# Kernel tuning notes

Measured on AMD Instinct MI355X. Metric: run time of the kernel, lower is better.

The kernel has to match this reference:

```python
import jax, jax.numpy as jnp
import numpy as np

N = 32768   # nodes
D = 16      # fixed in-degree (neighbors per node)
C = 128     # in_channels
H = 128     # hidden_channels (out of each SAGEConv)


def setup_inputs() -> dict:
    key = jax.random.key(0)
    ks = jax.random.split(key, 20)
    x = jax.random.normal(ks[0], (N, C), dtype=jnp.float32)
    # edges sorted by destination, exactly D neighbors per node (PyG
    # LSTMAggregation requires dst-sorted edge_index)
    src = jax.random.randint(ks[1], (N * D,), 0, N, dtype=jnp.int32)
    dst = jnp.repeat(jnp.arange(N, dtype=jnp.int32), D)
    edge_index = jnp.stack([src, dst])  # [2, E]

    s = 1.0 / np.sqrt(C)
    def mat(k, o, i):
        return jax.random.uniform(k, (o, i), jnp.float32, -s, s)
    def vec(k, o):
        return jax.random.uniform(k, (o,), jnp.float32, -s, s)

    inp = {"x": x, "edge_index": edge_index}
    for k0, base in [(2, "conv1"), (10, "conv2")]:
        inp[f"{base}_wih"] = mat(ks[k0 + 0], 4 * C, C)   # LSTM input weights
        inp[f"{base}_whh"] = mat(ks[k0 + 1], 4 * C, C)   # LSTM hidden weights
        inp[f"{base}_bih"] = vec(ks[k0 + 2], 4 * C)
        inp[f"{base}_bhh"] = vec(ks[k0 + 3], 4 * C)
        inp[f"{base}_wl"] = mat(ks[k0 + 4], H, C)        # lin_l (neighbor branch, has bias)
        inp[f"{base}_bl"] = vec(ks[k0 + 5], H)
        inp[f"{base}_wr"] = mat(ks[k0 + 6], H, C)        # lin_r (root branch, no bias)
    return inp


def _lstm_last(seq, wih, whh, bih, bhh):
    # seq: [D, N, C]. PyTorch LSTM, gate order (i, f, g, o).
    # PyG LSTMAggregation returns lstm(x)[0][:, -1] == hidden state at the
    # last (padded) timestep; here every node has exactly D real neighbors.
    n = seq.shape[1]
    h0 = jnp.zeros((n, wih.shape[0] // 4), seq.dtype)
    b = bih + bhh

    def step(carry, x_t):
        h, c = carry
        g = x_t @ wih.T + h @ whh.T + b            # [N, 4H]
        i, f, gg, o = jnp.split(g, 4, axis=-1)
        c = jax.nn.sigmoid(f) * c + jax.nn.sigmoid(i) * jnp.tanh(gg)
        h = jax.nn.sigmoid(o) * jnp.tanh(c)
        return (h, c), None

    (h, _), _ = jax.lax.scan(step, (h0, h0), seq)
    return h


def _sage_conv(x, src, wih, whh, bih, bhh, wl, bl, wr):
    n, c = x.shape
    d = src.shape[0] // n
    # dense neighbor batch [N, D, C]: edges are dst-sorted with fixed degree,
    # so the gather reshapes directly (== PyG to_dense_batch)
    msgs = x[src].reshape(n, d, c)
    aggr = _lstm_last(jnp.swapaxes(msgs, 0, 1), wih, whh, bih, bhh)  # [N, C]
    return aggr @ wl.T + bl + x @ wr.T


def reference(x, edge_index,
              conv1_wih, conv1_whh, conv1_bih, conv1_bhh, conv1_wl, conv1_bl, conv1_wr,
              conv2_wih, conv2_whh, conv2_bih, conv2_bhh, conv2_wl, conv2_bl, conv2_wr):
    src = edge_index[0]
    h = _sage_conv(x, src, conv1_wih, conv1_whh, conv1_bih, conv1_bhh,
                   conv1_wl, conv1_bl, conv1_wr)
    h = jax.nn.relu(h)
    out = _sage_conv(h, src, conv2_wih, conv2_whh, conv2_bih, conv2_bhh,
                     conv2_wl, conv2_bl, conv2_wr)
    return out
```

## Files before the change

### kernel.cpp

```cpp
#include <hip/hip_runtime.h>
#include <stdint.h>

#define NN 32768
#define DEG 16
#define CH 128
#define G4 512
#define MB 128
#define BUF 32768

typedef short bf16x8 __attribute__((ext_vector_type(8)));
typedef float f32x4 __attribute__((ext_vector_type(4)));
typedef unsigned short u16;
typedef u16 u16x8 __attribute__((ext_vector_type(8)));
typedef uint32_t u32;

#define L2E  1.4426950408889634f
#define L2E2 2.8853900817779268f

__device__ __forceinline__ u16 f2bf(float f) {
  union { float f; uint32_t u; } v; v.f = f;
  uint32_t u = v.u;
  return (u16)((u + 0x7FFFu + ((u >> 16) & 1u)) >> 16);
}
__device__ __forceinline__ float exp2f_fast(float x) {
#if __has_builtin(__builtin_amdgcn_exp2f)
  return __builtin_amdgcn_exp2f(x);
#else
  float r; asm("v_exp_f32 %0, %1" : "=v"(r) : "v"(x)); return r;
#endif
}
__device__ __forceinline__ float rcpf_fast(float x) {
#if __has_builtin(__builtin_amdgcn_rcpf)
  return __builtin_amdgcn_rcpf(x);
#else
  float r; asm("v_rcp_f32 %0, %1" : "=v"(r) : "v"(x)); return r;
#endif
}
__device__ __forceinline__ u32 cvtpk(float lo, float hi) {
  u32 r; asm("v_cvt_pk_bf16_f32 %0, %1, %2" : "=v"(r) : "v"(lo), "v"(hi));
  return r;
}

__global__ void k_cvt_bf16(const float* __restrict__ in, u16* __restrict__ out, int n8) {
  int i = blockIdx.x * blockDim.x + threadIdx.x;
  if (i >= n8) return;
  const float* pp = in + (size_t)i * 8;
  u16x8 o;
  #pragma unroll
  for (int j = 0; j < 8; ++j) o[j] = f2bf(pp[j]);
  *(u16x8*)(out + (size_t)i * 8) = o;
}

__global__ void k_pack_lstm(const float* __restrict__ wih, const float* __restrict__ whh,
                            const float* __restrict__ bih, const float* __restrict__ bhh,
                            u16* __restrict__ Wc, float* __restrict__ bs) {
  int idx = blockIdx.x * blockDim.x + threadIdx.x;
  int g = idx >> 8, k = idx & 255;
  int gate = g >> 7;
  float sc = (gate == 2) ? L2E2 : L2E;
  float v = (k < CH) ? wih[g * CH + k] : whh[g * CH + (k - CH)];
  Wc[g * 256 + k] = f2bf(v * sc);
  if (k == 0) bs[g] = (bih[g] + bhh[g]) * sc;
}

__global__ void k_pack_lin(const float* __restrict__ wl, const float* __restrict__ wr,
                           u16* __restrict__ W) {
  int idx = blockIdx.x * blockDim.x + threadIdx.x;
  int o = idx >> 8, k = idx & 255;
  float v = (k < CH) ? wl[o * CH + k] : wr[o * CH + (k - CH)];
  W[o * 256 + k] = f2bf(v);
}

__global__ __launch_bounds__(512, 2)
void k_gates(const u16* __restrict__ xin, const u16* __restrict__ Wc,
             u16* __restrict__ gx) {
  const int lane = threadIdx.x & 63;
  const int wave = threadIdx.x >> 6;
  const int l15 = lane & 15, lg = lane >> 4;
  const int nodeBase = blockIdx.x * 64;

  bf16x8 B[4][4];
  int cb[4];
  #pragma unroll
  for (int ct = 0; ct < 4; ++ct) {
    int j = (wave * 4 + ct) * 16 + l15;
    int wr = ((j & 3) << 7) + (j >> 2);
    cb[ct] = (j >> 2) * 8 + (j & 3) * 2;
    #pragma unroll
    for (int kt = 0; kt < 4; ++kt)
      B[ct][kt] = *(const bf16x8*)(Wc + wr * 256 + kt * 32 + lg * 8);
  }
  char* gxc = (char*)gx;
  const f32x4 zero4 = {0.f, 0.f, 0.f, 0.f};
  #pragma unroll
  for (int mt = 0; mt < 4; ++mt) {
    bf16x8 A[4];
    #pragma unroll
    for (int kt = 0; kt < 4; ++kt)
      A[kt] = *(const bf16x8*)(xin + (size_t)(nodeBase + mt * 16 + l15) * CH + kt * 32 + lg * 8);
    f32x4 acc[4] = { zero4, zero4, zero4, zero4 };
    #pragma unroll
    for (int kt = 0; kt < 4; ++kt)
      #pragma unroll
      for (int ct = 0; ct < 4; ++ct)
        acc[ct] = __builtin_amdgcn_mfma_f32_16x16x32_bf16(A[kt], B[ct][kt], acc[ct], 0, 0, 0);
    #pragma unroll
    for (int ct = 0; ct < 4; ++ct)
      #pragma unroll
      for (int q = 0; q < 4; ++q)
        *(u16*)(gxc + (size_t)(nodeBase + mt * 16 + lg * 4 + q) * 1024 + cb[ct]) =
            f2bf(acc[ct][q]);
  }
}

#define GXISSUE(m) do {                                                        \
    int4 sv_ = *(const int4*)(ldsc + sTr + (m) * 64);                          \
    gq[m][0] = *(const uint2*)(gxb + (((u32)sv_.x << 10) + gxoff));            \
    gq[m][1] = *(const uint2*)(gxb + (((u32)sv_.y << 10) + gxoff));            \
    gq[m][2] = *(const uint2*)(gxb + (((u32)sv_.z << 10) + gxoff));            \
    gq[m][3] = *(const uint2*)(gxb + (((u32)sv_.w << 10) + gxoff));            \
  } while (0)

__global__ __launch_bounds__(512, 2)
void k_lstm(const u16* __restrict__ gx, const int* __restrict__ src,
            const u16* __restrict__ Wc, const float* __restrict__ bs,
            u16* __restrict__ aggr) {
  __shared__ char lds[2 * 32768 + 8192];
  char* ldsc = lds;
  const int tid = threadIdx.x;
  const int lane = tid & 63;
  const int wave = tid >> 6;
  const int l15 = lane & 15;
  const int lg  = lane >> 4;
  const int nodeBase = blockIdx.x * MB;

  {
    int row = tid >> 2, tq = (tid & 3) * 4;
    int4 s4 = *(const int4*)(src + (size_t)(nodeBase + row) * DEG + tq);
    int b = 65536 + row * 4;
    *(int*)(ldsc + b + (tq + 0) * 512) = s4.x;
    *(int*)(ldsc + b + (tq + 1) * 512) = s4.y;
    *(int*)(ldsc + b + (tq + 2) * 512) = s4.z;
    *(int*)(ldsc + b + (tq + 3) * 512) = s4.w;
  }
  {
    int4 z = {0, 0, 0, 0};
    #pragma unroll
    for (int j = 0; j < 4; ++j) *(int4*)(ldsc + tid * 64 + j * 16) = z;
  }

  bf16x8 Wf[4][4];
  {
    const u16* wp = Wc + (wave * 16 + l15) * 256 + 128 + lg * 8;
    #pragma unroll
    for (int gt = 0; gt < 4; ++gt)
      #pragma unroll
      for (int kt = 0; kt < 4; ++kt)
        Wf[gt][kt] = *(const bf16x8*)(wp + gt * (CH * 256) + kt * 32);
  }
  f32x4 bias[4];
  #pragma unroll
  for (int gt = 0; gt < 4; ++gt) {
    float b = bs[gt * CH + wave * 16 + l15];
    bias[gt] = { b, b, b, b };
  }

  int aAr = l15 * 256 + ((lg * 16) ^ ((l15 & 7) << 4));
  int aBr = aAr ^ 64;
  const int hcol = (wave * 16 + l15) * 2;
  int hw0 = (lg * 4 + 0) * 256 + (hcol ^ ((((lg * 4) + 0) & 7) << 4)) + BUF;
  int hw1 = (lg * 4 + 1) * 256 + (hcol ^ ((((lg * 4) + 1) & 7) << 4)) + BUF;
  int hw2 = (lg * 4 + 2) * 256 + (hcol ^ ((((lg * 4) + 2) & 7) << 4)) + BUF;
  int hw3 = (lg * 4 + 3) * 256 + (hcol ^ ((((lg * 4) + 3) & 7) << 4)) + BUF;
  int sTr = 65536 + lg * 16;
  const u32 gxoff = (u32)(wave * 16 + l15) * 8;
  const char* gxb = (const char*)gx;
  u16* aggrp = aggr + (size_t)(nodeBase + lg * 4) * CH + wave * 16 + l15;

  float cst[8][4] = {{0.f}};
  f32x4 acc[2][4];

  __syncthreads();

  #pragma unroll 1
  for (int t = 0; t < DEG; ++t) {
    __syncthreads();
    uint2 gq[8][4];
    GXISSUE(0); GXISSUE(1); GXISSUE(2);
    #pragma unroll
    for (int mt = 0; mt < 8; ++mt) {
      const int pp = mt & 1;
      if (mt < 5) GXISSUE(mt + 3);
      __builtin_amdgcn_s_setprio(1);
      {
        const bf16x8 A0 = *(const bf16x8*)(ldsc + aAr + mt * 4096);
        const bf16x8 A1 = *(const bf16x8*)(ldsc + aBr + mt * 4096);
        const bf16x8 A2 = *(const bf16x8*)(ldsc + aAr + mt * 4096 + 128);
        const bf16x8 A3 = *(const bf16x8*)(ldsc + aBr + mt * 4096 + 128);
        #pragma unroll
        for (int gt = 0; gt < 4; ++gt)
          acc[pp][gt] = __builtin_amdgcn_mfma_f32_16x16x32_bf16(A0, Wf[gt][0], bias[gt], 0, 0, 0);
        #pragma unroll
        for (int gt = 0; gt < 4; ++gt)
          acc[pp][gt] = __builtin_amdgcn_mfma_f32_16x16x32_bf16(A1, Wf[gt][1], acc[pp][gt], 0, 0, 0);
        #pragma unroll
        for (int gt = 0; gt < 4; ++gt)
          acc[pp][gt] = __builtin_amdgcn_mfma_f32_16x16x32_bf16(A2, Wf[gt][2], acc[pp][gt], 0, 0, 0);
        #pragma unroll
        for (int gt = 0; gt < 4; ++gt)
          acc[pp][gt] = __builtin_amdgcn_mfma_f32_16x16x32_bf16(A3, Wf[gt][3], acc[pp][gt], 0, 0, 0);
      }
      __builtin_amdgcn_s_setprio(0);
      float hq[4];
      #pragma unroll
      for (int q = 0; q < 4; ++q) {
        float xi = __uint_as_float(gq[mt][q].x << 16);
        float xf = __uint_as_float(gq[mt][q].x & 0xFFFF0000u);
        float xg = __uint_as_float(gq[mt][q].y << 16);
        float xo = __uint_as_float(gq[mt][q].y & 0xFFFF0000u);
        float p0 = acc[pp][0][q] + xi;
        float p1 = acc[pp][1][q] + xf;
        float p2 = acc[pp][2][q] + xg;
        float p3 = acc[pp][3][q] + xo;
        float si = rcpf_fast(1.0f + exp2f_fast(-p0));
        float sf = rcpf_fast(1.0f + exp2f_fast(-p1));
        float so = rcpf_fast(1.0f + exp2f_fast(-p3));
        float gg = fmaf(-2.0f, rcpf_fast(1.0f + exp2f_fast(p2)), 1.0f);
        float c  = fmaf(sf, cst[mt][q], si * gg);
        cst[mt][q] = c;
        float tc = fmaf(-2.0f, rcpf_fast(1.0f + exp2f_fast(c * L2E2)), 1.0f);
        hq[q] = so * tc;
      }
      u32 hp0 = cvtpk(hq[0], hq[1]);
      u32 hp1 = cvtpk(hq[2], hq[3]);
      if (t != DEG - 1) {
        *(u16*)(ldsc + hw0 + mt * 4096) = (u16)hp0;
        *(u16*)(ldsc + hw1 + mt * 4096) = (u16)(hp0 >> 16);
        *(u16*)(ldsc + hw2 + mt * 4096) = (u16)hp1;
        *(u16*)(ldsc + hw3 + mt * 4096) = (u16)(hp1 >> 16);
      } else {
        u16* op_ = aggrp + mt * 16 * CH;
        op_[0 * CH] = (u16)hp0;
        op_[1 * CH] = (u16)(hp0 >> 16);
        op_[2 * CH] = (u16)hp1;
        op_[3 * CH] = (u16)(hp1 >> 16);
      }
    }
    aAr ^= BUF; aBr ^= BUF;
    hw0 ^= BUF; hw1 ^= BUF; hw2 ^= BUF; hw3 ^= BUF;
    sTr += 512;
  }
}

__global__ __launch_bounds__(256, 4)
void k_linear(const u16* __restrict__ aggr, const u16* __restrict__ xroot,
              const u16* __restrict__ W, const float* __restrict__ bl,
              u16* __restrict__ out_bf, float* __restrict__ out_f, int relu) {
  const int lane = threadIdx.x & 63;
  const int wave = threadIdx.x >> 6;
  const int l15 = lane & 15, lg = lane >> 4;
  const int rowBase = blockIdx.x * 64 + wave * 16;

  f32x4 acc[8];
  #pragma unroll
  for (int nt = 0; nt < 8; ++nt) {
    float b = bl[nt * 16 + l15];
    acc[nt] = { b, b, b, b };
  }
  #pragma unroll
  for (int kt = 0; kt < 8; ++kt) {
    const u16* ap = (kt < 4) ? (aggr  + (size_t)(rowBase + l15) * CH + kt * 32 + lg * 8)
                             : (xroot + (size_t)(rowBase + l15) * CH + (kt - 4) * 32 + lg * 8);
    bf16x8 A = *(const bf16x8*)ap;
    #pragma unroll
    for (int nt = 0; nt < 8; ++nt) {
      bf16x8 B = *(const bf16x8*)(W + (nt * 16 + l15) * 256 + kt * 32 + lg * 8);
      acc[nt] = __builtin_amdgcn_mfma_f32_16x16x32_bf16(A, B, acc[nt], 0, 0, 0);
    }
  }
  #pragma unroll
  for (int nt = 0; nt < 8; ++nt) {
    #pragma unroll
    for (int q = 0; q < 4; ++q) {
      float v = acc[nt][q];
      if (relu) v = fmaxf(v, 0.0f);
      int row = rowBase + lg * 4 + q;
      int col = nt * 16 + l15;
      if (out_bf) out_bf[(size_t)row * CH + col] = f2bf(v);
      else        out_f[(size_t)row * CH + col]  = v;
    }
  }
}

extern "C" void kernel_launch(void* const* d_in, const int* in_sizes, int n_in,
                              void* d_out, int out_size, void* d_ws, size_t ws_size,
                              hipStream_t stream) {
  (void)in_sizes; (void)n_in; (void)out_size; (void)ws_size;
  const float* x    = (const float*)d_in[0];
  const int*   ei   = (const int*)d_in[1];
  const float* w1ih = (const float*)d_in[2];
  const float* w1hh = (const float*)d_in[3];
  const float* b1ih = (const float*)d_in[4];
  const float* b1hh = (const float*)d_in[5];
  const float* w1l  = (const float*)d_in[6];
  const float* b1l  = (const float*)d_in[7];
  const float* w1r  = (const float*)d_in[8];
  const float* w2ih = (const float*)d_in[9];
  const float* w2hh = (const float*)d_in[10];
  const float* b2ih = (const float*)d_in[11];
  const float* b2hh = (const float*)d_in[12];
  const float* w2l  = (const float*)d_in[13];
  const float* b2l  = (const float*)d_in[14];
  const float* w2r  = (const float*)d_in[15];

  char* p = (char*)d_ws;
  u16* x_bf  = (u16*)p;  p += (size_t)NN * CH * 2;
  u16* h1_bf = (u16*)p;  p += (size_t)NN * CH * 2;
  u16* ag_bf = (u16*)p;  p += (size_t)NN * CH * 2;
  u16* Wc1   = (u16*)p;  p += G4 * 256 * 2;
  u16* Wc2   = (u16*)p;  p += G4 * 256 * 2;
  u16* Wl1   = (u16*)p;  p += CH * 256 * 2;
  u16* Wl2   = (u16*)p;  p += CH * 256 * 2;
  float* bs1 = (float*)p; p += G4 * 4;
  float* bs2 = (float*)p; p += G4 * 4;
  u16* Gx    = (u16*)p;  p += (size_t)NN * G4 * 2;

  k_cvt_bf16<<<(NN * CH / 8 + 255) / 256, 256, 0, stream>>>(x, x_bf, NN * CH / 8);
  k_pack_lstm<<<G4, 256, 0, stream>>>(w1ih, w1hh, b1ih, b1hh, Wc1, bs1);
  k_pack_lstm<<<G4, 256, 0, stream>>>(w2ih, w2hh, b2ih, b2hh, Wc2, bs2);
  k_pack_lin<<<CH, 256, 0, stream>>>(w1l, w1r, Wl1);
  k_pack_lin<<<CH, 256, 0, stream>>>(w2l, w2r, Wl2);

  k_gates<<<NN / 64, 512, 0, stream>>>(x_bf, Wc1, Gx);
  k_lstm<<<NN / MB, 512, 0, stream>>>(Gx, ei, Wc1, bs1, ag_bf);
  k_linear<<<NN / 64, 256, 0, stream>>>(ag_bf, x_bf, Wl1, b1l, h1_bf, nullptr, 1);
  k_gates<<<NN / 64, 512, 0, stream>>>(h1_bf, Wc2, Gx);
  k_lstm<<<NN / MB, 512, 0, stream>>>(Gx, ei, Wc2, bs2, ag_bf);
  k_linear<<<NN / 64, 256, 0, stream>>>(ag_bf, h1_bf, Wl2, b2l, nullptr, (float*)d_out, 0);
}
```

Measured before the change: 331.7 us.

## Halve LSTM block tile, raise occupancy, prefetch gate gathers across steps

The LSTM kernel now processes 64 nodes per block instead of 128, with half the LDS footprint and launch bounds raised to 4 blocks per SM. It also software-pipelines the gathered input-gate loads one step ahead, including across timesteps. The input-gate bias is folded into the gates GEMM so the per-step accumulator starts from the gathered gate values, and the five prep kernels are merged into a single launch. The aim is better latency hiding for the recurrent step and the random gathers. In exchange there is more register pressure and each block's weight-fragment load is amortized over fewer nodes.

```diff
diff --git a/kernel.cpp b/kernel.cpp
--- a/kernel.cpp
+++ b/kernel.cpp
@@ -4,9 +4,8 @@
 #define NN 32768
 #define DEG 16
 #define CH 128
-#define G4 512
-#define MB 128
-#define BUF 32768
+#define MB 64
+#define BUF 16384
 
 typedef short bf16x8 __attribute__((ext_vector_type(8)));
 typedef float f32x4 __attribute__((ext_vector_type(4)));
@@ -26,14 +25,14 @@
 #if __has_builtin(__builtin_amdgcn_exp2f)
   return __builtin_amdgcn_exp2f(x);
 #else
-  float r; asm("v_exp_f32 %0, %1" : "=v"(r) : "v"(x)); return r;
+  float r; asm volatile("v_exp_f32 %0, %1\n\ts_nop 0" : "=v"(r) : "v"(x)); return r;
 #endif
 }
 __device__ __forceinline__ float rcpf_fast(float x) {
 #if __has_builtin(__builtin_amdgcn_rcpf)
   return __builtin_amdgcn_rcpf(x);
 #else
-  float r; asm("v_rcp_f32 %0, %1" : "=v"(r) : "v"(x)); return r;
+  float r; asm volatile("v_rcp_f32 %0, %1\n\ts_nop 0" : "=v"(r) : "v"(x)); return r;
 #endif
 }
 __device__ __forceinline__ u32 cvtpk(float lo, float hi) {
@@ -41,64 +40,81 @@
   return r;
 }
 
-__global__ void k_cvt_bf16(const float* __restrict__ in, u16* __restrict__ out, int n8) {
-  int i = blockIdx.x * blockDim.x + threadIdx.x;
-  if (i >= n8) return;
-  const float* pp = in + (size_t)i * 8;
-  u16x8 o;
-  #pragma unroll
-  for (int j = 0; j < 8; ++j) o[j] = f2bf(pp[j]);
-  *(u16x8*)(out + (size_t)i * 8) = o;
-}
-
-__global__ void k_pack_lstm(const float* __restrict__ wih, const float* __restrict__ whh,
-                            const float* __restrict__ bih, const float* __restrict__ bhh,
-                            u16* __restrict__ Wc, float* __restrict__ bs) {
-  int idx = blockIdx.x * blockDim.x + threadIdx.x;
-  int g = idx >> 8, k = idx & 255;
-  int gate = g >> 7;
-  float sc = (gate == 2) ? L2E2 : L2E;
-  float v = (k < CH) ? wih[g * CH + k] : whh[g * CH + (k - CH)];
-  Wc[g * 256 + k] = f2bf(v * sc);
-  if (k == 0) bs[g] = (bih[g] + bhh[g]) * sc;
-}
-
-__global__ void k_pack_lin(const float* __restrict__ wl, const float* __restrict__ wr,
-                           u16* __restrict__ W) {
-  int idx = blockIdx.x * blockDim.x + threadIdx.x;
-  int o = idx >> 8, k = idx & 255;
-  float v = (k < CH) ? wl[o * CH + k] : wr[o * CH + (k - CH)];
-  W[o * 256 + k] = f2bf(v);
+__global__ void k_prep(const float* __restrict__ x, u16* __restrict__ x_bf,
+    const float* __restrict__ w1ih, const float* __restrict__ w1hh,
+    const float* __restrict__ b1ih, const float* __restrict__ b1hh,
+    u16* __restrict__ Wc1, float* __restrict__ bs1,
+    const float* __restrict__ w2ih, const float* __restrict__ w2hh,
+    const float* __restrict__ b2ih, const float* __restrict__ b2hh,
+    u16* __restrict__ Wc2, float* __restrict__ bs2,
+    const float* __restrict__ w1l, const float* __restrict__ w1r, u16* __restrict__ Wl1,
+    const float* __restrict__ w2l, const float* __restrict__ w2r, u16* __restrict__ Wl2) {
+  const int bid = blockIdx.x, tid = threadIdx.x;
+  {
+    int i = bid * 256 + tid;
+    const float* pp = x + (size_t)i * 8;
+    u16x8 o;
+    #pragma unroll
+    for (int j = 0; j < 8; ++j) o[j] = f2bf(pp[j]);
+    *(u16x8*)(x_bf + (size_t)i * 8) = o;
+  }
+  if (bid < 1024) {
+    const int b2 = bid >= 512;
+    const float* wih = b2 ? w2ih : w1ih;
+    const float* whh = b2 ? w2hh : w1hh;
+    const float* bih = b2 ? b2ih : b1ih;
+    const float* bhh = b2 ? b2hh : b1hh;
+    u16* Wc = b2 ? Wc2 : Wc1;
+    float* bsp = b2 ? bs2 : bs1;
+    int idx = (bid & 511) * 256 + tid;
+    int g = idx >> 8, k = idx & 255;
+    float sc = ((g >> 7) == 2) ? L2E2 : L2E;
+    float v = (k < CH) ? wih[g * CH + k] : whh[g * CH + (k - CH)];
+    Wc[g * 256 + k] = f2bf(v * sc);
+    if (k == 0) bsp[g] = (bih[g] + bhh[g]) * sc;
+  } else if (bid < 1280) {
+    const int b2 = bid >= 1152;
+    const float* wl = b2 ? w2l : w1l;
+    const float* wr = b2 ? w2r : w1r;
+    u16* W = b2 ? Wl2 : Wl1;
+    int idx = ((bid - 1024) & 127) * 256 + tid;
+    int o = idx >> 8, k = idx & 255;
+    float v = (k < CH) ? wl[o * CH + k] : wr[o * CH + (k - CH)];
+    W[o * 256 + k] = f2bf(v);
+  }
 }
 
 __global__ __launch_bounds__(512, 2)
 void k_gates(const u16* __restrict__ xin, const u16* __restrict__ Wc,
-             u16* __restrict__ gx) {
+             const float* __restrict__ bs, u16* __restrict__ gx) {
   const int lane = threadIdx.x & 63;
   const int wave = threadIdx.x >> 6;
   const int l15 = lane & 15, lg = lane >> 4;
   const int nodeBase = blockIdx.x * 64;
 
   bf16x8 B[4][4];
+  float bv[4];
   int cb[4];
   #pragma unroll
   for (int ct = 0; ct < 4; ++ct) {
     int j = (wave * 4 + ct) * 16 + l15;
     int wr = ((j & 3) << 7) + (j >> 2);
     cb[ct] = (j >> 2) * 8 + (j & 3) * 2;
+    bv[ct] = bs[wr];
     #pragma unroll
     for (int kt = 0; kt < 4; ++kt)
       B[ct][kt] = *(const bf16x8*)(Wc + wr * 256 + kt * 32 + lg * 8);
   }
   char* gxc = (char*)gx;
-  const f32x4 zero4 = {0.f, 0.f, 0.f, 0.f};
   #pragma unroll
   for (int mt = 0; mt < 4; ++mt) {
     bf16x8 A[4];
     #pragma unroll
     for (int kt = 0; kt < 4; ++kt)
       A[kt] = *(const bf16x8*)(xin + (size_t)(nodeBase + mt * 16 + l15) * CH + kt * 32 + lg * 8);
-    f32x4 acc[4] = { zero4, zero4, zero4, zero4 };
+    f32x4 acc[4];
+    #pragma unroll
+    for (int ct = 0; ct < 4; ++ct) acc[ct] = { bv[ct], bv[ct], bv[ct], bv[ct] };
     #pragma unroll
     for (int kt = 0; kt < 4; ++kt)
       #pragma unroll
@@ -113,20 +129,71 @@
   }
 }
 
-#define GXISSUE(m) do {                                                        \
-    int4 sv_ = *(const int4*)(ldsc + sTr + (m) * 64);                          \
-    gq[m][0] = *(const uint2*)(gxb + (((u32)sv_.x << 10) + gxoff));            \
-    gq[m][1] = *(const uint2*)(gxb + (((u32)sv_.y << 10) + gxoff));            \
-    gq[m][2] = *(const uint2*)(gxb + (((u32)sv_.z << 10) + gxoff));            \
-    gq[m][3] = *(const uint2*)(gxb + (((u32)sv_.w << 10) + gxoff));            \
+#define GXLD(SET, TOFF, M) do {                                                \
+    int4 sv_ = *(const int4*)(ldsc + sTr + ((TOFF) * 256 + (M) * 64));         \
+    SET[0] = *(const uint2*)(gxp + ((size_t)(u32)sv_.x << 10));                \
+    SET[1] = *(const uint2*)(gxp + ((size_t)(u32)sv_.y << 10));                \
+    SET[2] = *(const uint2*)(gxp + ((size_t)(u32)sv_.z << 10));                \
+    SET[3] = *(const uint2*)(gxp + ((size_t)(u32)sv_.w << 10));                \
   } while (0)
 
-__global__ __launch_bounds__(512, 2)
+#define MT_BODY(MT, G, ISSUE_STMT) do {                                        \
+  ISSUE_STMT;                                                                  \
+  f32x4 acg[4];                                                                \
+  _Pragma("unroll")                                                            \
+  for (int q = 0; q < 4; ++q) {                                                \
+    acg[0][q] = __uint_as_float((u32)G[q].x << 16);                            \
+    acg[1][q] = __uint_as_float(G[q].x & 0xFFFF0000u);                         \
+    acg[2][q] = __uint_as_float((u32)G[q].y << 16);                            \
+    acg[3][q] = __uint_as_float(G[q].y & 0xFFFF0000u);                         \
+  }                                                                            \
+  bf16x8 Aa[4];                                                                \
+  Aa[0] = *(const bf16x8*)(ldsc + aAr + (MT) * 4096);                          \
+  Aa[1] = *(const bf16x8*)(ldsc + aBr + (MT) * 4096);                          \
+  Aa[2] = *(const bf16x8*)(ldsc + aAr + (MT) * 4096 + 128);                    \
+  Aa[3] = *(const bf16x8*)(ldsc + aBr + (MT) * 4096 + 128);                    \
+  __builtin_amdgcn_s_setprio(1);                                               \
+  _Pragma("unroll")                                                            \
+  for (int kt = 0; kt < 4; ++kt)                                               \
+    _Pragma("unroll")                                                          \
+    for (int gt = 0; gt < 4; ++gt)                                             \
+      acg[gt] = __builtin_amdgcn_mfma_f32_16x16x32_bf16(Aa[kt], Wf[gt][kt],    \
+                                                        acg[gt], 0, 0, 0);     \
+  __builtin_amdgcn_s_setprio(0);                                               \
+  float hq[4];                                                                 \
+  _Pragma("unroll")                                                            \
+  for (int q = 0; q < 4; ++q) {                                                \
+    float si = rcpf_fast(1.0f + exp2f_fast(-acg[0][q]));                       \
+    float sf = rcpf_fast(1.0f + exp2f_fast(-acg[1][q]));                       \
+    float so = rcpf_fast(1.0f + exp2f_fast(-acg[3][q]));                       \
+    float gg = fmaf(-2.0f, rcpf_fast(1.0f + exp2f_fast(acg[2][q])), 1.0f);     \
+    float c  = fmaf(sf, cst[MT][q], si * gg);                                  \
+    cst[MT][q] = c;                                                            \
+    float tc = fmaf(-2.0f, rcpf_fast(1.0f + exp2f_fast(c * L2E2)), 1.0f);      \
+    hq[q] = so * tc;                                                           \
+  }                                                                            \
+  u32 hp0 = cvtpk(hq[0], hq[1]);                                               \
+  u32 hp1 = cvtpk(hq[2], hq[3]);                                               \
+  if (t != DEG - 1) {                                                          \
+    *(u16*)(ldsc + (hwB ^  0) + (MT) * 4096 +   0) = (u16)hp0;                 \
+    *(u16*)(ldsc + (hwB ^ 16) + (MT) * 4096 + 256) = (u16)(hp0 >> 16);         \
+    *(u16*)(ldsc + (hwB ^ 32) + (MT) * 4096 + 512) = (u16)hp1;                 \
+    *(u16*)(ldsc + (hwB ^ 48) + (MT) * 4096 + 768) = (u16)(hp1 >> 16);         \
+  } else {                                                                     \
+    u16* op_ = aggr + (size_t)(nodeBase + (MT) * 16 + lg * 4) * CH             \
+               + wave * 16 + l15;                                              \
+    op_[0 * CH] = (u16)hp0;                                                    \
+    op_[1 * CH] = (u16)(hp0 >> 16);                                            \
+    op_[2 * CH] = (u16)hp1;                                                    \
+    op_[3 * CH] = (u16)(hp1 >> 16);                                            \
+  }                                                                            \
+} while (0)
+
+__global__ __launch_bounds__(512, 4)
 void k_lstm(const u16* __restrict__ gx, const int* __restrict__ src,
-            const u16* __restrict__ Wc, const float* __restrict__ bs,
-            u16* __restrict__ aggr) {
-  __shared__ char lds[2 * 32768 + 8192];
-  char* ldsc = lds;
+            const u16* __restrict__ Wc, u16* __restrict__ aggr) {
+  __shared__ char ldsA[2 * BUF + 4096];
+  char* ldsc = ldsA;
   const int tid = threadIdx.x;
   const int lane = tid & 63;
   const int wave = tid >> 6;
@@ -135,18 +202,15 @@
   const int nodeBase = blockIdx.x * MB;
 
   {
-    int row = tid >> 2, tq = (tid & 3) * 4;
-    int4 s4 = *(const int4*)(src + (size_t)(nodeBase + row) * DEG + tq);
-    int b = 65536 + row * 4;
-    *(int*)(ldsc + b + (tq + 0) * 512) = s4.x;
-    *(int*)(ldsc + b + (tq + 1) * 512) = s4.y;
-    *(int*)(ldsc + b + (tq + 2) * 512) = s4.z;
-    *(int*)(ldsc + b + (tq + 3) * 512) = s4.w;
+    int row = tid >> 3, tq = (tid & 7) * 2;
+    int2 s2 = *(const int2*)(src + (size_t)(nodeBase + row) * DEG + tq);
+    *(int*)(ldsc + 2 * BUF + tq * 256 + row * 4)       = s2.x;
+    *(int*)(ldsc + 2 * BUF + (tq + 1) * 256 + row * 4) = s2.y;
   }
   {
     int4 z = {0, 0, 0, 0};
-    #pragma unroll
-    for (int j = 0; j < 4; ++j) *(int4*)(ldsc + tid * 64 + j * 16) = z;
+    *(int4*)(ldsc + tid * 32)      = z;
+    *(int4*)(ldsc + tid * 32 + 16) = z;
   }
 
   bf16x8 Wf[4][4];
@@ -158,97 +222,29 @@
       for (int kt = 0; kt < 4; ++kt)
         Wf[gt][kt] = *(const bf16x8*)(wp + gt * (CH * 256) + kt * 32);
   }
-  f32x4 bias[4];
-  #pragma unroll
-  for (int gt = 0; gt < 4; ++gt) {
-    float b = bs[gt * CH + wave * 16 + l15];
-    bias[gt] = { b, b, b, b };
-  }
 
   int aAr = l15 * 256 + ((lg * 16) ^ ((l15 & 7) << 4));
   int aBr = aAr ^ 64;
-  const int hcol = (wave * 16 + l15) * 2;
-  int hw0 = (lg * 4 + 0) * 256 + (hcol ^ ((((lg * 4) + 0) & 7) << 4)) + BUF;
-  int hw1 = (lg * 4 + 1) * 256 + (hcol ^ ((((lg * 4) + 1) & 7) << 4)) + BUF;
-  int hw2 = (lg * 4 + 2) * 256 + (hcol ^ ((((lg * 4) + 2) & 7) << 4)) + BUF;
-  int hw3 = (lg * 4 + 3) * 256 + (hcol ^ ((((lg * 4) + 3) & 7) << 4)) + BUF;
-  int sTr = 65536 + lg * 16;
-  const u32 gxoff = (u32)(wave * 16 + l15) * 8;
-  const char* gxb = (const char*)gx;
-  u16* aggrp = aggr + (size_t)(nodeBase + lg * 4) * CH + wave * 16 + l15;
-
-  float cst[8][4] = {{0.f}};
-  f32x4 acc[2][4];
+  int hwB = lg * 1024 + (((wave * 16 + l15) * 2) ^ ((lg & 1) << 6)) + BUF;
+  int sTr = 2 * BUF + lg * 16;
+  const char* gxp = (const char*)gx + (size_t)(wave * 16 + l15) * 8;
+
+  float cst[4][4] = {{0.f}};
 
   __syncthreads();
+  uint2 gq0[4], gq1[4], gq2[4], gq3[4];
+  GXLD(gq0, 0, 0);
 
   #pragma unroll 1
   for (int t = 0; t < DEG; ++t) {
+    GXLD(gq1, 0, 1);
+    MT_BODY(0, gq0, GXLD(gq2, 0, 2));
+    MT_BODY(1, gq1, GXLD(gq3, 0, 3));
+    MT_BODY(2, gq2, if (t != DEG - 1) GXLD(gq0, 1, 0));
+    MT_BODY(3, gq3, );
+    aAr ^= BUF; aBr ^= BUF; hwB ^= BUF;
+    sTr += 256;
     __syncthreads();
-    uint2 gq[8][4];
-    GXISSUE(0); GXISSUE(1); GXISSUE(2);
-    #pragma unroll
-    for (int mt = 0; mt < 8; ++mt) {
-      const int pp = mt & 1;
-      if (mt < 5) GXISSUE(mt + 3);
-      __builtin_amdgcn_s_setprio(1);
-      {
-        const bf16x8 A0 = *(const bf16x8*)(ldsc + aAr + mt * 4096);
-        const bf16x8 A1 = *(const bf16x8*)(ldsc + aBr + mt * 4096);
-        const bf16x8 A2 = *(const bf16x8*)(ldsc + aAr + mt * 4096 + 128);
-        const bf16x8 A3 = *(const bf16x8*)(ldsc + aBr + mt * 4096 + 128);
-        #pragma unroll
-        for (int gt = 0; gt < 4; ++gt)
-          acc[pp][gt] = __builtin_amdgcn_mfma_f32_16x16x32_bf16(A0, Wf[gt][0], bias[gt], 0, 0, 0);
-        #pragma unroll
-        for (int gt = 0; gt < 4; ++gt)
-          acc[pp][gt] = __builtin_amdgcn_mfma_f32_16x16x32_bf16(A1, Wf[gt][1], acc[pp][gt], 0, 0, 0);
-        #pragma unroll
-        for (int gt = 0; gt < 4; ++gt)
-          acc[pp][gt] = __builtin_amdgcn_mfma_f32_16x16x32_bf16(A2, Wf[gt][2], acc[pp][gt], 0, 0, 0);
-        #pragma unroll
-        for (int gt = 0; gt < 4; ++gt)
-          acc[pp][gt] = __builtin_amdgcn_mfma_f32_16x16x32_bf16(A3, Wf[gt][3], acc[pp][gt], 0, 0, 0);
-      }
-      __builtin_amdgcn_s_setprio(0);
-      float hq[4];
-      #pragma unroll
-      for (int q = 0; q < 4; ++q) {
-        float xi = __uint_as_float(gq[mt][q].x << 16);
-        float xf = __uint_as_float(gq[mt][q].x & 0xFFFF0000u);
-        float xg = __uint_as_float(gq[mt][q].y << 16);
-        float xo = __uint_as_float(gq[mt][q].y & 0xFFFF0000u);
-        float p0 = acc[pp][0][q] + xi;
-        float p1 = acc[pp][1][q] + xf;
-        float p2 = acc[pp][2][q] + xg;
-        float p3 = acc[pp][3][q] + xo;
-        float si = rcpf_fast(1.0f + exp2f_fast(-p0));
-        float sf = rcpf_fast(1.0f + exp2f_fast(-p1));
-        float so = rcpf_fast(1.0f + exp2f_fast(-p3));
-        float gg = fmaf(-2.0f, rcpf_fast(1.0f + exp2f_fast(p2)), 1.0f);
-        float c  = fmaf(sf, cst[mt][q], si * gg);
-        cst[mt][q] = c;
-        float tc = fmaf(-2.0f, rcpf_fast(1.0f + exp2f_fast(c * L2E2)), 1.0f);
-        hq[q] = so * tc;
-      }
-      u32 hp0 = cvtpk(hq[0], hq[1]);
-      u32 hp1 = cvtpk(hq[2], hq[3]);
-      if (t != DEG - 1) {
-        *(u16*)(ldsc + hw0 + mt * 4096) = (u16)hp0;
-        *(u16*)(ldsc + hw1 + mt * 4096) = (u16)(hp0 >> 16);
-        *(u16*)(ldsc + hw2 + mt * 4096) = (u16)hp1;
-        *(u16*)(ldsc + hw3 + mt * 4096) = (u16)(hp1 >> 16);
-      } else {
-        u16* op_ = aggrp + mt * 16 * CH;
-        op_[0 * CH] = (u16)hp0;
-        op_[1 * CH] = (u16)(hp0 >> 16);
-        op_[2 * CH] = (u16)hp1;
-        op_[3 * CH] = (u16)(hp1 >> 16);
-      }
-    }
-    aAr ^= BUF; aBr ^= BUF;
-    hw0 ^= BUF; hw1 ^= BUF; hw2 ^= BUF; hw3 ^= BUF;
-    sTr += 512;
   }
 }
 
@@ -317,24 +313,23 @@
   u16* x_bf  = (u16*)p;  p += (size_t)NN * CH * 2;
   u16* h1_bf = (u16*)p;  p += (size_t)NN * CH * 2;
   u16* ag_bf = (u16*)p;  p += (size_t)NN * CH * 2;
-  u16* Wc1   = (u16*)p;  p += G4 * 256 * 2;
-  u16* Wc2   = (u16*)p;  p += G4 * 256 * 2;
-  u16* Wl1   = (u16*)p;  p += CH * 256 * 2;
-  u16* Wl2   = (u16*)p;  p += CH * 256 * 2;
-  float* bs1 = (float*)p; p += G4 * 4;
-  float* bs2 = (float*)p; p += G4 * 4;
-  u16* Gx    = (u16*)p;  p += (size_t)NN * G4 * 2;
-
-  k_cvt_bf16<<<(NN * CH / 8 + 255) / 256, 256, 0, stream>>>(x, x_bf, NN * CH / 8);
-  k_pack_lstm<<<G4, 256, 0, stream>>>(w1ih, w1hh, b1ih, b1hh, Wc1, bs1);
-  k_pack_lstm<<<G4, 256, 0, stream>>>(w2ih, w2hh, b2ih, b2hh, Wc2, bs2);
-  k_pack_lin<<<CH, 256, 0, stream>>>(w1l, w1r, Wl1);
-  k_pack_lin<<<CH, 256, 0, stream>>>(w2l, w2r, Wl2);
-
-  k_gates<<<NN / 64, 512, 0, stream>>>(x_bf, Wc1, Gx);
-  k_lstm<<<NN / MB, 512, 0, stream>>>(Gx, ei, Wc1, bs1, ag_bf);
+  u16* Wc1   = (u16*)p;  p += (size_t)512 * 256 * 2;
+  u16* Wc2   = (u16*)p;  p += (size_t)512 * 256 * 2;
+  u16* Wl1   = (u16*)p;  p += (size_t)CH * 256 * 2;
+  u16* Wl2   = (u16*)p;  p += (size_t)CH * 256 * 2;
+  float* bs1 = (float*)p; p += 512 * 4;
+  float* bs2 = (float*)p; p += 512 * 4;
+  u16* Gx    = (u16*)p;  p += (size_t)NN * 512 * 2;
+
+  k_prep<<<2048, 256, 0, stream>>>(x, x_bf,
+      w1ih, w1hh, b1ih, b1hh, Wc1, bs1,
+      w2ih, w2hh, b2ih, b2hh, Wc2, bs2,
+      w1l, w1r, Wl1, w2l, w2r, Wl2);
+
+  k_gates<<<NN / 64, 512, 0, stream>>>(x_bf, Wc1, bs1, Gx);
+  k_lstm<<<NN / MB, 512, 0, stream>>>(Gx, ei, Wc1, ag_bf);
   k_linear<<<NN / 64, 256, 0, stream>>>(ag_bf, x_bf, Wl1, b1l, h1_bf, nullptr, 1);
-  k_gates<<<NN / 64, 512, 0, stream>>>(h1_bf, Wc2, Gx);
-  k_lstm<<<NN / MB, 512, 0, stream>>>(Gx, ei, Wc2, bs2, ag_bf);
+  k_gates<<<NN / 64, 512, 0, stream>>>(h1_bf, Wc2, bs2, Gx);
+  k_lstm<<<NN / MB, 512, 0, stream>>>(Gx, ei, Wc2, ag_bf);
   k_linear<<<NN / 64, 256, 0, stream>>>(ag_bf, h1_bf, Wl2, b2l, nullptr, (float*)d_out, 0);
 }
```

New measurement: 569.3 us. 1.72x slower.
